# Performance work log

Measured on AMD Instinct MI355X. Metric: run time of the kernel, lower is better.

## Reference

```python
import jax, jax.numpy as jnp
import numpy as np

GROUP_SIZE = 128  # vLLM machete default group size
ZERO_POINT = 8.0  # uint4b8: stored unsigned 4-bit, logical value = q - 8


def setup_inputs() -> dict:
    key = jax.random.key(0)
    k_a, k_b, k_s = jax.random.split(key, 3)
    M, K, N = 4096, 4096, 12288
    a = jax.random.normal(k_a, (M, K), dtype=jnp.float32)
    # int4 quantized weights stored as small ints in [0, 16)
    b_q = jax.random.randint(k_b, (K, N), 0, 16, dtype=jnp.int32)
    # per-group scales: one scale per (group of 128 rows of K) per output column
    scales = jax.random.uniform(k_s, (K // GROUP_SIZE, N), dtype=jnp.float32) * 0.02 + 0.001
    return {"a": a, "b_q": b_q, "scales": scales}


def reference(a, b_q, scales):
    K, N = b_q.shape
    G = K // GROUP_SIZE
    # dequantize: (q - 8) * group_scale, scale broadcast over each K-group
    b = (b_q.astype(jnp.float32) - ZERO_POINT).reshape(G, GROUP_SIZE, N)
    b = (b * scales[:, None, :]).reshape(K, N)  # [K, N] dequantized weights
    return a @ b  # [M, N]
```

## Files before the change

### kernel.cpp

```cpp
#include <hip/hip_runtime.h>
#include <hip/hip_bf16.h>
#include <stdint.h>

constexpr int Mdim = 4096;
constexpr int Kdim = 4096;
constexpr int Ndim = 12288;

constexpr int NKT = Kdim / 64;
constexpr int GM256 = Mdim / 256;
constexpr int GN256 = Ndim / 256;
constexpr int NWG256 = GM256 * GN256;
constexpr int GRID_M = Mdim / 128;
constexpr int GRID_N = Ndim / 128;
constexpr int NWG = GRID_M * GRID_N;

typedef float  f32x4   __attribute__((ext_vector_type(4)));
typedef __bf16 bf16x4v __attribute__((ext_vector_type(4)));
typedef __bf16 bf16x8v __attribute__((ext_vector_type(8)));
typedef int    i32x4   __attribute__((ext_vector_type(4)));
typedef unsigned short ushort8 __attribute__((ext_vector_type(8)));

typedef __attribute__((address_space(3))) uint32_t       lds_u32;
typedef __attribute__((address_space(1))) const uint32_t glb_u32;

__device__ __forceinline__ void gload16(const void* g, void* l) {
    __builtin_amdgcn_global_load_lds((glb_u32*)(uintptr_t)g,
                                     (lds_u32*)(uint32_t)(uintptr_t)l, 16, 0, 0);
}


__launch_bounds__(256)
__global__ void cvtA(const float* __restrict__ A, unsigned short* __restrict__ Aw) {
    int t = blockIdx.x * 256 + threadIdx.x;
    int r = t >> 9;
    int c = t & 511;
    const float* src = A + ((long)r << 12) + (c << 3);
    f32x4 v0 = *(const f32x4*)src;
    f32x4 v1 = *(const f32x4*)(src + 4);
    bf16x8v o;
#pragma unroll
    for (int j = 0; j < 4; ++j) { o[j] = (__bf16)v0[j]; o[4 + j] = (__bf16)v1[j]; }
    int ks = c & 3;
    int cp = (c & ~3) | (ks ^ ((r >> 1) & 3));
    *(bf16x8v*)(Aw + ((long)r << 12) + (cp << 3)) = o;
}

__launch_bounds__(256)
__global__ void deqB(const int* __restrict__ Bq, const float* __restrict__ S,
                     unsigned short* __restrict__ Bw) {
    __shared__ unsigned short lt[64][72];
    int kb = blockIdx.x & 63;
    int nb = blockIdx.x >> 6;
    int k0 = kb << 6, n0 = nb << 6;
    int tid = threadIdx.x;
    int g = k0 >> 7;
    int nq = (tid & 15) << 2;
    f32x4 sc = *(const f32x4*)(S + (long)g * Ndim + n0 + nq);
#pragma unroll
    for (int p = 0; p < 4; ++p) {
        int kk = (p << 4) + (tid >> 4);
        i32x4 q = *(const i32x4*)(Bq + (long)(k0 + kk) * Ndim + n0 + nq);
#pragma unroll
        for (int j = 0; j < 4; ++j) {
            float v = ((float)q[j] - 8.f) * sc[j];
            lt[nq + j][kk] = __builtin_bit_cast(unsigned short, (__bf16)v);
        }
    }
    __syncthreads();
#pragma unroll
    for (int h = 0; h < 2; ++h) {
        int cidx = tid + (h << 8);
        int n = cidx >> 3, sidx = cidx & 7;
        int kh = sidx >> 2, ks = sidx & 3;
        int ksp = ks ^ ((n >> 1) & 3);
        ushort8 v = *(const ushort8*)&lt[n][sidx << 3];
        *(ushort8*)(Bw + (long)(n0 + n) * Kdim + k0 + kh * 32 + ksp * 8) = v;
    }
}

__launch_bounds__(512, 2)
__global__ void gemm256(const unsigned short* __restrict__ Aw,
                        const unsigned short* __restrict__ Bw,
                        float* __restrict__ C) {
    extern __shared__ unsigned char ldsbuf[];

    const int tid  = threadIdx.x;
    const int lane = tid & 63;
    const int w    = tid >> 6;
    const int wr   = w >> 2, wc = w & 3;
    const int fr   = lane & 15;
    const int ks   = lane >> 4;

    const int bid = blockIdx.x;
    const int xcd = bid & 7;
    const int loc = bid >> 3;
    const int pn  = loc >> 4;
    const int tm  = loc & 15;
    const int tn  = xcd * 6 + pn;
    const int brow = tm << 8, bcol = tn << 8;

    const unsigned char* pA = (const unsigned char*)Aw
        + (size_t)(brow + (tid >> 2)) * 8192 + (size_t)(tid & 3) * 16;
    const unsigned char* pA2 = pA + (size_t)128 * 8192;
    const unsigned char* pB = (const unsigned char*)Bw
        + (size_t)(bcol + (tid >> 2)) * 8192 + (size_t)(tid & 3) * 16;
    const unsigned char* pB2 = pB + (size_t)128 * 8192;
    const int ldw = w << 10;

    int offA[8][2], offB[4][2];
#pragma unroll
    for (int am = 0; am < 8; ++am)
#pragma unroll
        for (int kh = 0; kh < 2; ++kh) {
            int rowL = wr * 128 + am * 16 + fr;
            offA[am][kh] = (kh << 14) + rowL * 64 + ((ks ^ ((rowL >> 1) & 3)) << 4);
        }
#pragma unroll
    for (int n = 0; n < 4; ++n)
#pragma unroll
        for (int kh = 0; kh < 2; ++kh) {
            int colL = wc * 64 + n * 16 + fr;
            offB[n][kh] = (kh << 14) + colL * 64 + ((ks ^ ((colL >> 1) & 3)) << 4);
        }

    f32x4 acc[8][4];
#pragma unroll
    for (int m = 0; m < 8; ++m)
#pragma unroll
        for (int n = 0; n < 4; ++n) acc[m][n] = (f32x4){0.f, 0.f, 0.f, 0.f};

#define STG_A(DSTB, OFF)                                                      \
    gload16(pA  + (OFF), ldsbuf + (DSTB) + ldw);                              \
    gload16(pA2 + (OFF), ldsbuf + (DSTB) + ldw + 8192);
#define STG_B(DSTB, OFF)                                                      \
    gload16(pB  + (OFF), ldsbuf + (DSTB) + 32768 + ldw);                      \
    gload16(pB2 + (OFF), ldsbuf + (DSTB) + 32768 + ldw + 8192);

#define TILE(BUF, O1, O2, STG1, STG2, VM)                                     \
    {                                                                         \
        unsigned char* sAc = ldsbuf + ((BUF) << 16);                          \
        unsigned char* sBc = sAc + 32768;                                     \
        bf16x8v aF[8], bF[4];                                                 \
        _Pragma("unroll") for (int m = 0; m < 8; ++m)                         \
            aF[m] = *(const bf16x8v*)(sAc + offA[m][0]);                      \
        _Pragma("unroll") for (int n = 0; n < 4; ++n)                         \
            bF[n] = *(const bf16x8v*)(sBc + offB[n][0]);                      \
        if (STG1) { STG_A(((1 - (BUF)) << 16) + (1 << 14), O1)                \
                    STG_B(((1 - (BUF)) << 16) + (1 << 14), O1) }              \
        __builtin_amdgcn_s_setprio(1);                                        \
        _Pragma("unroll") for (int m = 0; m < 8; ++m)                         \
            _Pragma("unroll") for (int n = 0; n < 4; ++n)                     \
                acc[m][n] = __builtin_amdgcn_mfma_f32_16x16x32_bf16(          \
                    aF[m], bF[n], acc[m][n], 0, 0, 0);                        \
        __builtin_amdgcn_s_setprio(0);                                        \
        __builtin_amdgcn_s_barrier();                                         \
        __builtin_amdgcn_sched_barrier(0);   \
        _Pragma("unroll") for (int m = 0; m < 8; ++m)                         \
            aF[m] = *(const bf16x8v*)(sAc + offA[m][1]);                      \
        _Pragma("unroll") for (int n = 0; n < 4; ++n)                         \
            bF[n] = *(const bf16x8v*)(sBc + offB[n][1]);                      \
        if (STG2) { STG_A(((BUF) << 16), O2)                                  \
                    STG_B(((BUF) << 16), O2) }                                \
        __builtin_amdgcn_s_setprio(1);                                        \
        _Pragma("unroll") for (int m = 0; m < 8; ++m)                         \
            _Pragma("unroll") for (int n = 0; n < 4; ++n)                     \
                acc[m][n] = __builtin_amdgcn_mfma_f32_16x16x32_bf16(          \
                    aF[m], bF[n], acc[m][n], 0, 0, 0);                        \
        __builtin_amdgcn_s_setprio(0);                                        \
        asm volatile("s_waitcnt vmcnt(" #VM ")" ::: "memory");                \
        __builtin_amdgcn_s_barrier();                                         \
    }

    STG_A(0, 0)                 STG_B(0, 0)
    STG_A((1 << 14), 64)        STG_B((1 << 14), 64)
    STG_A((1 << 16), 128)       STG_B((1 << 16), 128)
    asm volatile("s_waitcnt vmcnt(4)" ::: "memory");
    __builtin_amdgcn_s_barrier();

    for (int it = 0; it < 31; ++it) {
        TILE(0, 192, 256, 1, 1, 4)
        TILE(1, 320, 384, 1, 1, 4)
        pA += 256; pA2 += 256; pB += 256; pB2 += 256;
    }
    TILE(0, 192, 0, 1, 0, 0)
    {
        unsigned char* sAc = ldsbuf + (1 << 16);
        unsigned char* sBc = sAc + 32768;
#pragma unroll
        for (int kh = 0; kh < 2; ++kh) {
            bf16x8v aF[8], bF[4];
#pragma unroll
            for (int m = 0; m < 8; ++m) aF[m] = *(const bf16x8v*)(sAc + offA[m][kh]);
#pragma unroll
            for (int n = 0; n < 4; ++n) bF[n] = *(const bf16x8v*)(sBc + offB[n][kh]);
#pragma unroll
            for (int m = 0; m < 8; ++m)
#pragma unroll
                for (int n = 0; n < 4; ++n)
                    acc[m][n] = __builtin_amdgcn_mfma_f32_16x16x32_bf16(
                        aF[m], bF[n], acc[m][n], 0, 0, 0);
        }
    }

#pragma unroll
    for (int m = 0; m < 8; ++m) {
        int row = brow + wr * 128 + m * 16 + ks * 4;
#pragma unroll
        for (int n = 0; n < 4; ++n) {
            int col = bcol + wc * 64 + n * 16 + fr;
            f32x4 v = acc[m][n];
            float* cp = C + (size_t)row * Ndim + col;
#pragma unroll
            for (int r = 0; r < 4; ++r) cp[(size_t)r * Ndim] = v[r];
        }
    }
#undef TILE
#undef STG_B
#undef STG_A
}

__launch_bounds__(256, 3)
__global__ void gemm_bf16(const unsigned short* __restrict__ Aw,
                          const unsigned short* __restrict__ Bw,
                          float* __restrict__ C) {
    __shared__ unsigned char sA[128 * 64 * 2];
    __shared__ unsigned char sB[128 * 64 * 2];

    const int tid  = threadIdx.x;
    const int lane = tid & 63;
    const int w    = tid >> 6;

    const int bid   = blockIdx.x;
    const int x     = bid & 7;
    const int local = bid >> 3;
    const int pn    = local >> 5;
    const int tm    = local & 31;
    const int tn    = x * 12 + pn;
    const int brow  = tm << 7;
    const int bcol  = tn << 7;

    const unsigned char* ga[4];
    const unsigned char* gb[4];
#pragma unroll
    for (int i = 0; i < 4; ++i) {
        int c = (w << 8) + (i << 6) + lane;
        int r = c >> 3, s = c & 7;
        ga[i] = (const unsigned char*)Aw + (long)(brow + r) * 8192 + (s << 4);
        gb[i] = (const unsigned char*)Bw + (long)(bcol + r) * 8192 + (s << 4);
    }

    const int fr = lane & 15;
    const int ks = lane >> 4;
    const int wr = w >> 1, wc = w & 1;
    int ra[4][2], rb[4][2];
#pragma unroll
    for (int m = 0; m < 4; ++m)
#pragma unroll
        for (int kk = 0; kk < 2; ++kk) {
            int r_a = wr * 64 + m * 16 + fr;
            int r_b = wc * 64 + m * 16 + fr;
            ra[m][kk] = (r_a << 7) + (kk << 6) + ((ks ^ ((r_a >> 1) & 3)) << 4);
            rb[m][kk] = (r_b << 7) + (kk << 6) + ((ks ^ ((r_b >> 1) & 3)) << 4);
        }

    f32x4 acc[4][4];
#pragma unroll
    for (int m = 0; m < 4; ++m)
#pragma unroll
        for (int n = 0; n < 4; ++n) acc[m][n] = (f32x4){0.f, 0.f, 0.f, 0.f};

    for (int kt = 0; kt < NKT; ++kt) {
#pragma unroll
        for (int i = 0; i < 4; ++i) {
            gload16(ga[i], sA + (((w << 2) + i) << 10));
            gload16(gb[i], sB + (((w << 2) + i) << 10));
            ga[i] += 128;
            gb[i] += 128;
        }
        __syncthreads();

#pragma unroll
        for (int kk = 0; kk < 2; ++kk) {
            bf16x8v af[4], bf[4];
#pragma unroll
            for (int m = 0; m < 4; ++m) af[m] = *(const bf16x8v*)(sA + ra[m][kk]);
#pragma unroll
            for (int n = 0; n < 4; ++n) bf[n] = *(const bf16x8v*)(sB + rb[n][kk]);
#pragma unroll
            for (int m = 0; m < 4; ++m)
#pragma unroll
                for (int n = 0; n < 4; ++n)
                    acc[m][n] = __builtin_amdgcn_mfma_f32_16x16x32_bf16(af[m], bf[n], acc[m][n], 0, 0, 0);
        }
        __syncthreads();
    }

#pragma unroll
    for (int m = 0; m < 4; ++m) {
        int row = brow + wr * 64 + m * 16 + ks * 4;
#pragma unroll
        for (int n = 0; n < 4; ++n) {
            int col = bcol + wc * 64 + n * 16 + fr;
            f32x4 v = acc[m][n];
            float* cp = C + (long)row * Ndim + col;
#pragma unroll
            for (int r = 0; r < 4; ++r) cp[(long)r * Ndim] = v[r];
        }
    }
}

__device__ __forceinline__ int swz_f(int row, int kbyte) {
    int s = kbyte >> 4;
    int f = s ^ ((row ^ (row >> 2)) & 7);
    return (row << 7) + (f << 4) + (kbyte & 15);
}

__launch_bounds__(256, 2)
__global__ void machete_fused(const float* __restrict__ A,
                              const int* __restrict__ Bq,
                              const float* __restrict__ S,
                              float* __restrict__ C) {
    __shared__ unsigned char sA[128 * 64 * 2];
    __shared__ unsigned char sB[128 * 64 * 2];

    const int tid = threadIdx.x;
    const int bid = blockIdx.x;
    const int sid = (bid & 7) * (NWG / 8) + (bid >> 3);
    const int tm = sid / GRID_N;
    const int tn = sid % GRID_N;
    const int brow = tm * 128;
    const int bcol = tn * 128;

    const int a_row0 = tid >> 4;
    const int a_kb   = tid & 15;
    const int b_kb = tid >> 4;
    const int b_nb = tid & 15;

    int aw[8];
#pragma unroll
    for (int i = 0; i < 8; ++i) aw[i] = swz_f(a_row0 + 16 * i, a_kb * 8);
    int bw[2][4];
#pragma unroll
    for (int i = 0; i < 2; ++i)
#pragma unroll
        for (int j = 0; j < 4; ++j) bw[i][j] = swz_f(4 * b_nb + 64 * i + j, b_kb * 8);

    const int lane = tid & 63;
    const int w  = tid >> 6;
    const int wr = w >> 1, wc = w & 1;
    const int fr = lane & 15;
    const int ks = lane >> 4;
    int ar[4][2], br[4][2];
#pragma unroll
    for (int m = 0; m < 4; ++m)
#pragma unroll
        for (int kk = 0; kk < 2; ++kk) {
            ar[m][kk] = swz_f(wr * 64 + m * 16 + fr, kk * 64 + ks * 16);
            br[m][kk] = swz_f(wc * 64 + m * 16 + fr, kk * 64 + ks * 16);
        }

    const float* Ap = A + (long)brow * Kdim;
    const int*   Bp = Bq + bcol;

    f32x4 aregs[8];
    i32x4 bregs[2][4];
    f32x4 sregs[2];

#pragma unroll
    for (int i = 0; i < 8; ++i)
        aregs[i] = *(const f32x4*)(Ap + (long)(a_row0 + 16 * i) * Kdim + a_kb * 4);
#pragma unroll
    for (int i = 0; i < 2; ++i) {
#pragma unroll
        for (int r = 0; r < 4; ++r)
            bregs[i][r] = *(const i32x4*)(Bp + (long)(b_kb * 4 + r) * Ndim + 4 * b_nb + 64 * i);
        sregs[i] = *(const f32x4*)(S + bcol + 4 * b_nb + 64 * i);
    }

    f32x4 acc[4][4];
#pragma unroll
    for (int m = 0; m < 4; ++m)
#pragma unroll
        for (int n = 0; n < 4; ++n) acc[m][n] = (f32x4){0.f, 0.f, 0.f, 0.f};

    for (int kt = 0; kt < NKT; ++kt) {
#pragma unroll
        for (int i = 0; i < 8; ++i) {
            f32x4 v = aregs[i];
            bf16x4v p;
            p[0] = (__bf16)v[0]; p[1] = (__bf16)v[1];
            p[2] = (__bf16)v[2]; p[3] = (__bf16)v[3];
            *(bf16x4v*)(sA + aw[i]) = p;
        }
#pragma unroll
        for (int i = 0; i < 2; ++i) {
            f32x4 sc = sregs[i];
#pragma unroll
            for (int j = 0; j < 4; ++j) {
                float scj = sc[j];
                float nm8 = -8.f * scj;
                bf16x4v p;
#pragma unroll
                for (int r = 0; r < 4; ++r) {
                    float v = (float)bregs[i][r][j] * scj + nm8;
                    p[r] = (__bf16)v;
                }
                *(bf16x4v*)(sB + bw[i][j]) = p;
            }
        }
        __syncthreads();

        if (kt + 1 < NKT) {
            const float* Ap2 = Ap + (kt + 1) * 64;
            const int*   Bp2 = Bq + bcol + (long)((kt + 1) * 64) * Ndim;
            const float* Sp2 = S + (long)((kt + 1) >> 1) * Ndim + bcol;
#pragma unroll
            for (int i = 0; i < 8; ++i)
                aregs[i] = *(const f32x4*)(Ap2 + (long)(a_row0 + 16 * i) * Kdim + a_kb * 4);
#pragma unroll
            for (int i = 0; i < 2; ++i) {
#pragma unroll
                for (int r = 0; r < 4; ++r)
                    bregs[i][r] = *(const i32x4*)(Bp2 + (long)(b_kb * 4 + r) * Ndim + 4 * b_nb + 64 * i);
                sregs[i] = *(const f32x4*)(Sp2 + 4 * b_nb + 64 * i);
            }
        }

#pragma unroll
        for (int kk = 0; kk < 2; ++kk) {
            bf16x8v af[4], bfv[4];
#pragma unroll
            for (int m = 0; m < 4; ++m) af[m] = *(const bf16x8v*)(sA + ar[m][kk]);
#pragma unroll
            for (int n = 0; n < 4; ++n) bfv[n] = *(const bf16x8v*)(sB + br[n][kk]);
#pragma unroll
            for (int m = 0; m < 4; ++m)
#pragma unroll
                for (int n = 0; n < 4; ++n)
                    acc[m][n] = __builtin_amdgcn_mfma_f32_16x16x32_bf16(af[m], bfv[n], acc[m][n], 0, 0, 0);
        }
        __syncthreads();
    }

#pragma unroll
    for (int m = 0; m < 4; ++m) {
        int row = brow + wr * 64 + m * 16 + ks * 4;
#pragma unroll
        for (int n = 0; n < 4; ++n) {
            int col = bcol + wc * 64 + n * 16 + fr;
            f32x4 v = acc[m][n];
            float* cp = C + (long)row * Ndim + col;
#pragma unroll
            for (int r = 0; r < 4; ++r) cp[(long)r * Ndim] = v[r];
        }
    }
}

extern "C" void kernel_launch(void* const* d_in, const int* in_sizes, int n_in,
                              void* d_out, int out_size, void* d_ws, size_t ws_size,
                              hipStream_t stream) {
    const float* A  = (const float*)d_in[0];
    const int*   Bq = (const int*)d_in[1];
    const float* S  = (const float*)d_in[2];
    float* C = (float*)d_out;

    const size_t a_elems = (size_t)Mdim * Kdim;
    const size_t b_elems = (size_t)Ndim * Kdim;
    const size_t need = (a_elems + b_elems) * sizeof(unsigned short);

    if (ws_size >= need) {
        unsigned short* Aw = (unsigned short*)d_ws;
        unsigned short* Bw = Aw + a_elems;
        hipLaunchKernelGGL(cvtA, dim3((Mdim * Kdim / 8) / 256), dim3(256), 0, stream, A, Aw);
        hipLaunchKernelGGL(deqB, dim3((Kdim / 64) * (Ndim / 64)), dim3(256), 0, stream, Bq, S, Bw);
        hipError_t e = hipFuncSetAttribute(
            reinterpret_cast<const void*>(gemm256),
            hipFuncAttributeMaxDynamicSharedMemorySize, 131072);
        if (e == hipSuccess) {
            hipLaunchKernelGGL(gemm256, dim3(NWG256), dim3(512), 131072, stream, Aw, Bw, C);
        } else {
            hipLaunchKernelGGL(gemm_bf16, dim3(NWG), dim3(256), 0, stream, Aw, Bw, C);
        }
    } else {
        hipLaunchKernelGGL(machete_fused, dim3(NWG), dim3(256), 0, stream, A, Bq, S, C);
    }
}
```

Baseline: 468.3 us.

## Switch GEMM main loop to simple full-tile double buffering

Replaces the staggered half-tile prefetch schedule, where each half of the next buffer is staged at a different point and guarded by a mid-tile barrier with partial vmcnt waits, with a plain double-buffer scheme. Each tile now issues all global loads for the other buffer at its start, loads both K-halves' fragments into separate registers, and waits on vmcnt(0) at its end. This removes one barrier per tile and simplifies the epilogue. In exchange the loads have less lead time and a full drain every tile, and register pressure rises from the extra fragment arrays.

Measured after the change: 477.7 us. 2.0% more time.

```diff
diff --git a/kernel.cpp b/kernel.cpp
--- a/kernel.cpp
+++ b/kernel.cpp
@@ -136,71 +136,53 @@
     gload16(pB  + (OFF), ldsbuf + (DSTB) + 32768 + ldw);                      \
     gload16(pB2 + (OFF), ldsbuf + (DSTB) + 32768 + ldw + 8192);
 
-#define TILE(BUF, O1, O2, STG1, STG2, VM)                                     \
+#define TILE(BUF, OFF, STG)                                                   \
     {                                                                         \
         unsigned char* sAc = ldsbuf + ((BUF) << 16);                          \
         unsigned char* sBc = sAc + 32768;                                     \
-        bf16x8v aF[8], bF[4];                                                 \
+        bf16x8v a0[8], b0[4], a1[8], b1[4];                                   \
         _Pragma("unroll") for (int m = 0; m < 8; ++m)                         \
-            aF[m] = *(const bf16x8v*)(sAc + offA[m][0]);                      \
+            a0[m] = *(const bf16x8v*)(sAc + offA[m][0]);                      \
         _Pragma("unroll") for (int n = 0; n < 4; ++n)                         \
-            bF[n] = *(const bf16x8v*)(sBc + offB[n][0]);                      \
-        if (STG1) { STG_A(((1 - (BUF)) << 16) + (1 << 14), O1)                \
-                    STG_B(((1 - (BUF)) << 16) + (1 << 14), O1) }              \
+            b0[n] = *(const bf16x8v*)(sBc + offB[n][0]);                      \
+        if (STG) {                                                            \
+            STG_A(((1 - (BUF)) << 16), OFF)                                   \
+            STG_B(((1 - (BUF)) << 16), OFF)                                   \
+            STG_A(((1 - (BUF)) << 16) + (1 << 14), (OFF) + 64)                \
+            STG_B(((1 - (BUF)) << 16) + (1 << 14), (OFF) + 64)                \
+        }                                                                     \
         __builtin_amdgcn_s_setprio(1);                                        \
         _Pragma("unroll") for (int m = 0; m < 8; ++m)                         \
             _Pragma("unroll") for (int n = 0; n < 4; ++n)                     \
                 acc[m][n] = __builtin_amdgcn_mfma_f32_16x16x32_bf16(          \
-                    aF[m], bF[n], acc[m][n], 0, 0, 0);                        \
+                    a0[m], b0[n], acc[m][n], 0, 0, 0);                        \
         __builtin_amdgcn_s_setprio(0);                                        \
-        __builtin_amdgcn_s_barrier();                                         \
-        __builtin_amdgcn_sched_barrier(0);   \
         _Pragma("unroll") for (int m = 0; m < 8; ++m)                         \
-            aF[m] = *(const bf16x8v*)(sAc + offA[m][1]);                      \
+            a1[m] = *(const bf16x8v*)(sAc + offA[m][1]);                      \
         _Pragma("unroll") for (int n = 0; n < 4; ++n)                         \
-            bF[n] = *(const bf16x8v*)(sBc + offB[n][1]);                      \
-        if (STG2) { STG_A(((BUF) << 16), O2)                                  \
-                    STG_B(((BUF) << 16), O2) }                                \
+            b1[n] = *(const bf16x8v*)(sBc + offB[n][1]);                      \
         __builtin_amdgcn_s_setprio(1);                                        \
         _Pragma("unroll") for (int m = 0; m < 8; ++m)                         \
             _Pragma("unroll") for (int n = 0; n < 4; ++n)                     \
                 acc[m][n] = __builtin_amdgcn_mfma_f32_16x16x32_bf16(          \
-                    aF[m], bF[n], acc[m][n], 0, 0, 0);                        \
+                    a1[m], b1[n], acc[m][n], 0, 0, 0);                        \
         __builtin_amdgcn_s_setprio(0);                                        \
-        asm volatile("s_waitcnt vmcnt(" #VM ")" ::: "memory");                \
+        asm volatile("s_waitcnt vmcnt(0)" ::: "memory");                      \
         __builtin_amdgcn_s_barrier();                                         \
     }
 
-    STG_A(0, 0)                 STG_B(0, 0)
-    STG_A((1 << 14), 64)        STG_B((1 << 14), 64)
-    STG_A((1 << 16), 128)       STG_B((1 << 16), 128)
-    asm volatile("s_waitcnt vmcnt(4)" ::: "memory");
+    STG_A(0, 0)          STG_B(0, 0)
+    STG_A((1 << 14), 64) STG_B((1 << 14), 64)
+    asm volatile("s_waitcnt vmcnt(0)" ::: "memory");
     __builtin_amdgcn_s_barrier();
 
     for (int it = 0; it < 31; ++it) {
-        TILE(0, 192, 256, 1, 1, 4)
-        TILE(1, 320, 384, 1, 1, 4)
+        TILE(0, 128, 1)
+        TILE(1, 256, 1)
         pA += 256; pA2 += 256; pB += 256; pB2 += 256;
     }
-    TILE(0, 192, 0, 1, 0, 0)
-    {
-        unsigned char* sAc = ldsbuf + (1 << 16);
-        unsigned char* sBc = sAc + 32768;
-#pragma unroll
-        for (int kh = 0; kh < 2; ++kh) {
-            bf16x8v aF[8], bF[4];
-#pragma unroll
-            for (int m = 0; m < 8; ++m) aF[m] = *(const bf16x8v*)(sAc + offA[m][kh]);
-#pragma unroll
-            for (int n = 0; n < 4; ++n) bF[n] = *(const bf16x8v*)(sBc + offB[n][kh]);
-#pragma unroll
-            for (int m = 0; m < 8; ++m)
-#pragma unroll
-                for (int n = 0; n < 4; ++n)
-                    acc[m][n] = __builtin_amdgcn_mfma_f32_16x16x32_bf16(
-                        aF[m], bF[n], acc[m][n], 0, 0, 0);
-        }
-    }
+    TILE(0, 128, 1)
+    TILE(1, 0, 0)
 
 #pragma unroll
     for (int m = 0; m < 8; ++m) {
```
